# Kernel optimization log

Hardware: AMD Instinct MI355X
Metric: run time of the kernel (lower is better)

## Reference

```python
import jax, jax.numpy as jnp
import numpy as np

S = 16          # spatial_size (adaptive pool output per dim)
EPS = 1e-8      # torch.cosine_similarity eps

def _avg_pool3d(x, s):
    # exact adaptive avg pool when D,H,W divisible by s
    B, C, D, H, W = x.shape
    kd, kh, kw = D // s, H // s, W // s
    x = x.reshape(B, C, s, kd, s, kh, s, kw)
    return x.mean(axis=(3, 5, 7))  # (B, C, s, s, s)

def _flatten_rows(x):
    # (B,C,s,s,s) -> (B*s^3, C), matching view+transpose+flatten
    B, C = x.shape[0], x.shape[1]
    return x.reshape(B, C, -1).transpose(0, 2, 1).reshape(-1, C)

def _cos_sim_matrix(a):
    # pairwise cosine similarity via normalize + GEMM
    norms = jnp.maximum(jnp.linalg.norm(a, axis=-1, keepdims=True), EPS)
    an = a / norms
    return an @ an.T  # (N, N)

def setup_inputs() -> dict:
    key = jax.random.key(0)
    k1, k2 = jax.random.split(key)
    shape = (2, 32, 64, 64, 64)
    p1 = jax.random.normal(k1, shape, dtype=jnp.float32)
    p2 = jax.random.normal(k2, shape, dtype=jnp.float32)
    return {"p1": p1, "p2": p2}

def reference(p1, p2):
    aa = _flatten_rows(_avg_pool3d(p1, S))  # (N, C), N = B*S^3
    bb = _flatten_rows(_avg_pool3d(p2, S))
    sim_a = _cos_sim_matrix(aa)
    sim_b = _cos_sim_matrix(bb)
    return jnp.mean((sim_a - sim_b) ** 2)  # MSELoss
```

## Files before the change

kernel.cpp:

```cpp
#include <hip/hip_runtime.h>
#include <hip/hip_bf16.h>


#define HW   4096
#define DHW  262144
#define NROW 8192
#define C    32

__global__ __launch_bounds__(256) void pool_norm_kernel(
    const float* __restrict__ p1, const float* __restrict__ p2,
    float* __restrict__ An, float* __restrict__ Bn)
{
    const int bid = blockIdx.x;
    const int y = bid & 15;
    const int z = (bid >> 4) & 15;
    const int b = bid >> 8;

    const float* __restrict__ src = (blockIdx.y == 0) ? p1 : p2;
    float* __restrict__ dst       = (blockIdx.y == 0) ? An : Bn;

    const int tid = threadIdx.x;
    const int x  = tid & 15;
    const int c0 = tid >> 4;

    __shared__ float pool[C][16];
    __shared__ float inv_norm[16];

    float pooled[2];
    #pragma unroll
    for (int cc = 0; cc < 2; ++cc) {
        const int c = c0 + cc * 16;
        const float* base = src + (size_t)(b * C + c) * DHW
                                + (4 * z) * HW + (4 * y) * 64 + 4 * x;
        float s = 0.f;
        #pragma unroll
        for (int dz = 0; dz < 4; ++dz) {
            #pragma unroll
            for (int dy = 0; dy < 4; ++dy) {
                const float4 v = *reinterpret_cast<const float4*>(base + dz * HW + dy * 64);
                s += (v.x + v.y) + (v.z + v.w);
            }
        }
        pooled[cc] = s * (1.0f / 64.0f);
        pool[c][x] = pooled[cc];
    }
    __syncthreads();

    if (tid < 16) {
        float ss = 0.f;
        #pragma unroll
        for (int c = 0; c < C; ++c) { const float v = pool[c][tid]; ss += v * v; }
        inv_norm[tid] = 1.0f / fmaxf(sqrtf(ss), 1e-8f);
    }
    __syncthreads();

    const int row = ((b * 16 + z) * 16 + y) * 16 + x;
    const float inv = inv_norm[x];
    #pragma unroll
    for (int cc = 0; cc < 2; ++cc) {
        const int c = c0 + cc * 16;
        dst[(size_t)row * C + c] = pooled[cc] * inv;
    }
}

__global__ __launch_bounds__(256) void gram_kernel(
    const float* __restrict__ An, const float* __restrict__ Bn,
    float* __restrict__ G)
{
    const int tid = threadIdx.x;
    const int k  = tid >> 3;
    const int l4 = (tid & 7) * 4;

    __shared__ float As[32 * C];
    __shared__ float Bs[32 * C];

    float gaa[4] = {0.f, 0.f, 0.f, 0.f};
    float gab[4] = {0.f, 0.f, 0.f, 0.f};
    float gbb[4] = {0.f, 0.f, 0.f, 0.f};

    const int row0 = blockIdx.x * 64;
    for (int t = 0; t < 2; ++t) {
        const int r = row0 + t * 32;
        reinterpret_cast<float4*>(As)[tid] =
            reinterpret_cast<const float4*>(An + (size_t)r * C)[tid];
        reinterpret_cast<float4*>(Bs)[tid] =
            reinterpret_cast<const float4*>(Bn + (size_t)r * C)[tid];
        __syncthreads();

        #pragma unroll
        for (int i = 0; i < 32; ++i) {
            const float a_k = As[i * C + k];
            const float b_k = Bs[i * C + k];
            const float4 a_l = *reinterpret_cast<const float4*>(&As[i * C + l4]);
            const float4 b_l = *reinterpret_cast<const float4*>(&Bs[i * C + l4]);
            gaa[0] += a_k * a_l.x;  gaa[1] += a_k * a_l.y;
            gaa[2] += a_k * a_l.z;  gaa[3] += a_k * a_l.w;
            gab[0] += a_k * b_l.x;  gab[1] += a_k * b_l.y;
            gab[2] += a_k * b_l.z;  gab[3] += a_k * b_l.w;
            gbb[0] += b_k * b_l.x;  gbb[1] += b_k * b_l.y;
            gbb[2] += b_k * b_l.z;  gbb[3] += b_k * b_l.w;
        }
        __syncthreads();
    }

    float* Gaa = G;
    float* Gab = G + 1024;
    float* Gbb = G + 2048;
    #pragma unroll
    for (int j = 0; j < 4; ++j) {
        atomicAdd(&Gaa[k * C + l4 + j], gaa[j]);
        atomicAdd(&Gab[k * C + l4 + j], gab[j]);
        atomicAdd(&Gbb[k * C + l4 + j], gbb[j]);
    }
}

__global__ __launch_bounds__(1024) void finalize_kernel(
    const float* __restrict__ G, float* __restrict__ out)
{
    const int t = threadIdx.x;
    const float gaa = G[t];
    const float gab = G[1024 + t];
    const float gbb = G[2048 + t];
    float v = gaa * gaa + gbb * gbb - 2.f * gab * gab;

    __shared__ float red[16];
    #pragma unroll
    for (int off = 32; off > 0; off >>= 1) v += __shfl_down(v, off);
    if ((t & 63) == 0) red[t >> 6] = v;
    __syncthreads();
    if (t < 16) {
        float w = red[t];
        #pragma unroll
        for (int off = 8; off > 0; off >>= 1) w += __shfl_down(w, off);
        if (t == 0) out[0] = w / ((float)NROW * (float)NROW);
    }
}

extern "C" void kernel_launch(void* const* d_in, const int* in_sizes, int n_in,
                              void* d_out, int out_size, void* d_ws, size_t ws_size,
                              hipStream_t stream) {
    const float* p1 = (const float*)d_in[0];
    const float* p2 = (const float*)d_in[1];
    float* out = (float*)d_out;

    float* An = (float*)d_ws;
    float* Bn = An + (size_t)NROW * C;
    float* G  = Bn + (size_t)NROW * C;

    hipMemsetAsync(G, 0, 3 * 1024 * sizeof(float), stream);

    dim3 g1(512, 2);
    pool_norm_kernel<<<g1, 256, 0, stream>>>(p1, p2, An, Bn);
    gram_kernel<<<128, 256, 0, stream>>>(An, Bn, G);
    finalize_kernel<<<1, 1024, 0, stream>>>(G, out);
}
```

Measured before the change: 163.7 us.

## Restructure pooling for contiguous reads and move normalization into gram kernel

The pooling kernel now assigns each block one (array, batch, channel, z-slab) and reads 16 contiguous KB of input with fully coalesced float4 loads, reducing with shuffles instead of scattered 4-float strided reads across channels. Because a block no longer holds all channels of a row, the row normalization moves into the gram kernel, which computes each row's norm via lane shuffles when it loads a tile. The pooled output writes become strided scalar stores (one channel per row), which may be less efficient, and the gram kernel does a small amount of extra work.

```diff
diff --git a/kernel.cpp b/kernel.cpp
--- a/kernel.cpp
+++ b/kernel.cpp
@@ -7,64 +7,50 @@
 #define NROW 8192
 #define C    32
 
-__global__ __launch_bounds__(256) void pool_norm_kernel(
+__global__ __launch_bounds__(256) void pool_kernel(
     const float* __restrict__ p1, const float* __restrict__ p2,
-    float* __restrict__ An, float* __restrict__ Bn)
+    float* __restrict__ Pa, float* __restrict__ Pb)
 {
     const int bid = blockIdx.x;
-    const int y = bid & 15;
-    const int z = (bid >> 4) & 15;
-    const int b = bid >> 8;
+    const int zp  = bid & 15;
+    const int c   = (bid >> 4) & 31;
+    const int b   = (bid >> 9) & 1;
+    const int arr = bid >> 10;
 
-    const float* __restrict__ src = (blockIdx.y == 0) ? p1 : p2;
-    float* __restrict__ dst       = (blockIdx.y == 0) ? An : Bn;
+    const float* __restrict__ src = arr ? p2 : p1;
+    float* __restrict__ dst       = arr ? Pb : Pa;
 
-    const int tid = threadIdx.x;
-    const int x  = tid & 15;
-    const int c0 = tid >> 4;
+    const float4* __restrict__ base = reinterpret_cast<const float4*>(
+        src + (size_t)(b * C + c) * DHW + (size_t)(zp * 4) * HW);
 
-    __shared__ float pool[C][16];
-    __shared__ float inv_norm[16];
+    const int tid  = threadIdx.x;
+    const int lane = tid & 63;
+    const int w    = tid >> 6;
 
-    float pooled[2];
+    __shared__ float pool[256];
+
     #pragma unroll
-    for (int cc = 0; cc < 2; ++cc) {
-        const int c = c0 + cc * 16;
-        const float* base = src + (size_t)(b * C + c) * DHW
-                                + (4 * z) * HW + (4 * y) * 64 + 4 * x;
+    for (int j = 0; j < 4; ++j) {
         float s = 0.f;
         #pragma unroll
         for (int dz = 0; dz < 4; ++dz) {
-            #pragma unroll
-            for (int dy = 0; dy < 4; ++dy) {
-                const float4 v = *reinterpret_cast<const float4*>(base + dz * HW + dy * 64);
-                s += (v.x + v.y) + (v.z + v.w);
-            }
+            const int p = j + 4 * dz;
+            const float4 v = base[p * 256 + tid];
+            s += (v.x + v.y) + (v.z + v.w);
         }
-        pooled[cc] = s * (1.0f / 64.0f);
-        pool[c][x] = pooled[cc];
+        s += __shfl_xor(s, 16);
+        s += __shfl_xor(s, 32);
+        const int yp = (4 * j + w) & 15;
+        if (lane < 16) pool[yp * 16 + lane] = s * (1.0f / 64.0f);
     }
     __syncthreads();
 
-    if (tid < 16) {
-        float ss = 0.f;
-        #pragma unroll
-        for (int c = 0; c < C; ++c) { const float v = pool[c][tid]; ss += v * v; }
-        inv_norm[tid] = 1.0f / fmaxf(sqrtf(ss), 1e-8f);
-    }
-    __syncthreads();
-
-    const int row = ((b * 16 + z) * 16 + y) * 16 + x;
-    const float inv = inv_norm[x];
-    #pragma unroll
-    for (int cc = 0; cc < 2; ++cc) {
-        const int c = c0 + cc * 16;
-        dst[(size_t)row * C + c] = pooled[cc] * inv;
-    }
+    const int n = b * 4096 + zp * 256 + tid;
+    dst[(size_t)n * C + c] = pool[tid];
 }
 
 __global__ __launch_bounds__(256) void gram_kernel(
-    const float* __restrict__ An, const float* __restrict__ Bn,
+    const float* __restrict__ Pa, const float* __restrict__ Pb,
     float* __restrict__ G)
 {
     const int tid = threadIdx.x;
@@ -81,10 +67,20 @@
     const int row0 = blockIdx.x * 64;
     for (int t = 0; t < 2; ++t) {
         const int r = row0 + t * 32;
-        reinterpret_cast<float4*>(As)[tid] =
-            reinterpret_cast<const float4*>(An + (size_t)r * C)[tid];
-        reinterpret_cast<float4*>(Bs)[tid] =
-            reinterpret_cast<const float4*>(Bn + (size_t)r * C)[tid];
+        float4 va = reinterpret_cast<const float4*>(Pa + (size_t)r * C)[tid];
+        float4 vb = reinterpret_cast<const float4*>(Pb + (size_t)r * C)[tid];
+
+        float ssa = va.x*va.x + va.y*va.y + va.z*va.z + va.w*va.w;
+        float ssb = vb.x*vb.x + vb.y*vb.y + vb.z*vb.z + vb.w*vb.w;
+        ssa += __shfl_xor(ssa, 1); ssa += __shfl_xor(ssa, 2); ssa += __shfl_xor(ssa, 4);
+        ssb += __shfl_xor(ssb, 1); ssb += __shfl_xor(ssb, 2); ssb += __shfl_xor(ssb, 4);
+        const float inva = 1.0f / fmaxf(sqrtf(ssa), 1e-8f);
+        const float invb = 1.0f / fmaxf(sqrtf(ssb), 1e-8f);
+        va.x *= inva; va.y *= inva; va.z *= inva; va.w *= inva;
+        vb.x *= invb; vb.y *= invb; vb.z *= invb; vb.w *= invb;
+
+        reinterpret_cast<float4*>(As)[tid] = va;
+        reinterpret_cast<float4*>(Bs)[tid] = vb;
         __syncthreads();
 
         #pragma unroll
@@ -143,14 +139,13 @@
     const float* p2 = (const float*)d_in[1];
     float* out = (float*)d_out;
 
-    float* An = (float*)d_ws;
-    float* Bn = An + (size_t)NROW * C;
-    float* G  = Bn + (size_t)NROW * C;
+    float* Pa = (float*)d_ws;
+    float* Pb = Pa + (size_t)NROW * C;
+    float* G  = Pb + (size_t)NROW * C;
 
     hipMemsetAsync(G, 0, 3 * 1024 * sizeof(float), stream);
 
-    dim3 g1(512, 2);
-    pool_norm_kernel<<<g1, 256, 0, stream>>>(p1, p2, An, Bn);
-    gram_kernel<<<128, 256, 0, stream>>>(An, Bn, G);
+    pool_kernel<<<2048, 256, 0, stream>>>(p1, p2, Pa, Pb);
+    gram_kernel<<<128, 256, 0, stream>>>(Pa, Pb, G);
     finalize_kernel<<<1, 1024, 0, stream>>>(G, out);
 }
```

Measured after the change: 167.6 us. 1.02x slower.
